# Performance work log

Hardware: AMD Instinct MI355X
Metric: run time of the kernel (lower is better)

The kernel has to match this reference:

```python
import jax, jax.numpy as jnp
import numpy as np

B, S, DIN, DOUT, H = 4, 2048, 512, 512, 8
DH = DOUT // H
EPS = 1e-5


def _conv_bn(x, conv_w, conv_b, bn_gamma, bn_beta, bn_mean, bn_var):
    # x: [B, S, DIN] -> permute to [B, DIN, S] like torch
    xc = jnp.transpose(x, (0, 2, 1))
    y = jax.lax.conv_general_dilated(
        xc, conv_w, window_strides=(1,), padding=[(3, 3)],
        dimension_numbers=('NCH', 'OIH', 'NCH'))  # [B, DOUT, S]
    y = y + conv_b[None, :, None]
    # BatchNorm1d in eval mode: normalize per channel with running stats
    inv = jax.lax.rsqrt(bn_var + EPS)
    y = (y - bn_mean[None, :, None]) * (inv * bn_gamma)[None, :, None] + bn_beta[None, :, None]
    return jnp.transpose(y, (0, 2, 1))  # back to [B, S, DOUT]


def setup_inputs() -> dict:
    key = jax.random.key(0)
    ks = jax.random.split(key, 4)
    return {
        'q': jax.random.normal(ks[0], (B, S, DIN), dtype=jnp.float32),
        'k': jax.random.normal(ks[1], (B, S, DIN), dtype=jnp.float32),
        'v': jax.random.normal(ks[2], (B, S, DIN), dtype=jnp.float32),
        'conv_w': jax.random.normal(ks[3], (DOUT, DIN, 7), dtype=jnp.float32) * 0.02,
        'conv_b': jnp.zeros((DOUT,), jnp.float32),
        'bn_gamma': jnp.ones((DOUT,), jnp.float32),
        'bn_beta': jnp.zeros((DOUT,), jnp.float32),
        'bn_mean': jnp.zeros((DOUT,), jnp.float32),
        'bn_var': jnp.ones((DOUT,), jnp.float32),
        'ln_gamma': jnp.ones((DOUT,), jnp.float32),
        'ln_beta': jnp.zeros((DOUT,), jnp.float32),
    }


def reference(q, k, v, conv_w, conv_b, bn_gamma, bn_beta, bn_mean, bn_var,
              ln_gamma, ln_beta):
    # shared conv+BN preproc applied to q, k, v, then split into heads [B,S,H,DH]
    qh = _conv_bn(q, conv_w, conv_b, bn_gamma, bn_beta, bn_mean, bn_var).reshape(B, S, H, DH)
    kh = _conv_bn(k, conv_w, conv_b, bn_gamma, bn_beta, bn_mean, bn_var).reshape(B, S, H, DH)
    vh = _conv_bn(v, conv_w, conv_b, bn_gamma, bn_beta, bn_mean, bn_var).reshape(B, S, H, DH)
    # full QK^T score matrix, scaled, softmax, times V (mask is None)
    scores = jnp.einsum('bqhd,bkhd->bhqk', qh, kh) * (1.0 / np.sqrt(DH).astype(np.float32))
    probs = jax.nn.softmax(scores, axis=-1)
    out = jnp.einsum('bhqk,bkhd->bqhd', probs, vh).reshape(B, S, DOUT)
    # dropout(p=0) is identity; final LayerNorm over feature dim
    mu = jnp.mean(out, axis=-1, keepdims=True)
    var = jnp.mean(jnp.square(out - mu), axis=-1, keepdims=True)
    return (out - mu) * jax.lax.rsqrt(var + EPS) * ln_gamma + ln_beta
```

## Files before the change

kernel.cpp:

```cpp
#include <hip/hip_runtime.h>
#include <hip/hip_bf16.h>


#define B_ 4
#define S_ 2048
#define DIN_ 512
#define DOUT_ 512
#define H_ 8
#define DH_ 64
#define EPS_ 1e-5f
#define SP_ 2054

using bf16x8 = __attribute__((ext_vector_type(8))) short;
using f32x4  = __attribute__((ext_vector_type(4))) float;

__device__ __forceinline__ unsigned short f2bf(float x) {
    union { float f; unsigned u; } v; v.f = x;
    unsigned r = v.u + 0x7FFF + ((v.u >> 16) & 1);
    return (unsigned short)(r >> 16);
}

__device__ __forceinline__ unsigned cvt2(float lo, float hi) {
    unsigned r;
    asm("v_cvt_pk_bf16_f32 %0, %1, %2" : "=v"(r) : "v"(lo), "v"(hi));
    return r;
}

__device__ __forceinline__ float fexp2(float x) {
    float r;
    asm("v_exp_f32 %0, %1" : "=v"(r) : "v"(x));
    return r;
}

__device__ __forceinline__ float bf2f(unsigned short u) {
    union { unsigned u; float f; } v; v.u = ((unsigned)u) << 16;
    return v.f;
}

typedef __attribute__((address_space(1))) const unsigned int GU32;
typedef __attribute__((address_space(3))) unsigned int LU32;
__device__ __forceinline__ void gl_lds16(const void* g, void* l) {
    __builtin_amdgcn_global_load_lds((GU32*)g, (LU32*)l, 16, 0, 0);
}

__global__ void cast_x(const float* __restrict__ q, const float* __restrict__ k,
                       const float* __restrict__ v, unsigned short* __restrict__ xb) {
    int i = blockIdx.x * 256 + threadIdx.x;
    int row = i >> 6;
    int cin = (i & 63) * 8;
    int tb = row / SP_;
    int pr = row - tb * SP_;
    int tensor = tb >> 2;
    int b = tb & 3;
    unsigned short* dst = xb + (size_t)row * DIN_ + cin;
    if (pr < 3 || pr >= SP_ - 3) {
        *reinterpret_cast<uint4*>(dst) = make_uint4(0, 0, 0, 0);
    } else {
        const float* src = (tensor == 0 ? q : (tensor == 1 ? k : v)) +
                           ((size_t)b * S_ + (pr - 3)) * DIN_ + cin;
        float4 a0 = *reinterpret_cast<const float4*>(src);
        float4 a1 = *reinterpret_cast<const float4*>(src + 4);
        uint4 o;
        o.x = cvt2(a0.x, a0.y); o.y = cvt2(a0.z, a0.w);
        o.z = cvt2(a1.x, a1.y); o.w = cvt2(a1.z, a1.w);
        *reinterpret_cast<uint4*>(dst) = o;
    }
}

__global__ void prep_w(const float* __restrict__ w, const float* __restrict__ cb,
                       const float* __restrict__ gamma, const float* __restrict__ beta,
                       const float* __restrict__ mean, const float* __restrict__ var,
                       unsigned short* __restrict__ w_eff, float* __restrict__ b_eff) {
    int gid = blockIdx.x * blockDim.x + threadIdx.x;
    if (gid < DOUT_) {
        float sc = gamma[gid] * rsqrtf(var[gid] + EPS_);
        b_eff[gid] = (cb[gid] - mean[gid]) * sc + beta[gid];
    }
    int total = 7 * DOUT_ * DIN_;
    for (int i = gid; i < total; i += gridDim.x * blockDim.x) {
        int t = i / (DOUT_ * DIN_);
        int rem = i - t * (DOUT_ * DIN_);
        int co = rem >> 9;
        int ci = rem & 511;
        float sc = gamma[co] * rsqrtf(var[co] + EPS_);
        w_eff[i] = f2bf(w[(co * DIN_ + ci) * 7 + t] * sc);
    }
}

__global__ __launch_bounds__(256, 3) void conv_bn(
        const unsigned short* __restrict__ xb,
        const unsigned short* __restrict__ w_eff,
        const float* __restrict__ b_eff,
        unsigned short* __restrict__ out3) {
    __shared__ alignas(16) unsigned short As[2][192 * 32];
    __shared__ alignas(16) unsigned short Bs[3][128 * 32];

    int orig = blockIdx.x;
    int bid = (orig & 7) * 96 + (orig >> 3);
    int tensor = bid >> 8;
    int rem = bid & 255;
    int batch = rem >> 6;
    int stile = (rem >> 2) & 15;
    int cotile = rem & 3;
    int s0 = stile * 128;
    int co0 = cotile * 128;

    const unsigned short* xp = xb + (size_t)(tensor * 4 + batch) * SP_ * DIN_;
    unsigned short* out = out3 + (size_t)tensor * (B_ * S_ * DOUT_) +
                          (size_t)batch * S_ * DOUT_;

    const int tid = threadIdx.x;
    const int l = tid & 63;
    const int wv = tid >> 6;
    const int g = l >> 4;
    const int c16 = l & 15;
    const int wrow = (wv >> 1) * 64;
    const int wcol = (wv & 1) * 64;

    const int dr4 = l >> 2;
    const int sch = ((l & 3) ^ ((l >> 3) & 3)) << 3;

#define STAGE_A(cc, buf) do {                                                   \
        _Pragma("unroll")                                                       \
        for (int j = 0; j < 3; ++j) {                                           \
            int r0 = (wv * 3 + j) * 16;                                         \
            int rs = r0 + dr4; if (rs > 133) rs = 133;                          \
            gl_lds16(xp + (size_t)(s0 + rs) * DIN_ + (cc) * 32 + sch,           \
                     &As[buf][r0 * 32]);                                        \
        }                                                                       \
    } while (0)

#define STAGE_B(cc, t, buf) do {                                                \
        const unsigned short* wp = w_eff + (size_t)(t) * (DOUT_ * DIN_) +       \
                                   (cc) * 32;                                   \
        _Pragma("unroll")                                                       \
        for (int j = 0; j < 2; ++j) {                                           \
            int r0 = (wv * 2 + j) * 16;                                         \
            gl_lds16(wp + (size_t)(co0 + r0 + dr4) * DIN_ + sch,                \
                     &Bs[buf][r0 * 32]);                                        \
        }                                                                       \
    } while (0)

    f32x4 acc[4][4] = {};

    STAGE_A(0, 0);
    STAGE_B(0, 0, 0);
    int bcur = 0;

    for (int cc = 0; cc < 16; ++cc) {
        const int ca = cc & 1;
        for (int t = 0; t < 7; ++t) {
            int bnext = (bcur == 2) ? 0 : bcur + 1;
            if (t < 6) {
                STAGE_B(cc, t + 1, bnext);
                asm volatile("s_waitcnt vmcnt(2)" ::: "memory");
            } else if (cc < 15) {
                STAGE_B(cc + 1, 0, bnext);
                STAGE_A(cc + 1, ca ^ 1);
                asm volatile("s_waitcnt vmcnt(5)" ::: "memory");
            } else {
                asm volatile("s_waitcnt vmcnt(0)" ::: "memory");
            }
            __builtin_amdgcn_s_barrier();

            const unsigned short* Ab = &As[ca][0];
            const unsigned short* Bb = &Bs[bcur][0];
            bf16x8 af[4], bfv[4];
#pragma unroll
            for (int m = 0; m < 4; ++m) {
                int r = wrow + m * 16 + c16 + t;
                af[m] = *reinterpret_cast<const bf16x8*>(
                    &Ab[r * 32 + ((g ^ ((r >> 1) & 3)) << 3)]);
            }
#pragma unroll
            for (int n = 0; n < 4; ++n) {
                int rb = wcol + n * 16 + c16;
                bfv[n] = *reinterpret_cast<const bf16x8*>(
                    &Bb[rb * 32 + ((g ^ ((rb >> 1) & 3)) << 3)]);
            }
            __builtin_amdgcn_s_setprio(1);
#pragma unroll
            for (int m = 0; m < 4; ++m)
#pragma unroll
                for (int n = 0; n < 4; ++n)
                    acc[m][n] = __builtin_amdgcn_mfma_f32_16x16x32_bf16(
                        af[m], bfv[n], acc[m][n], 0, 0, 0);
            __builtin_amdgcn_s_setprio(0);
            bcur = bnext;
        }
    }

    float osc = (tensor == 0) ? 0.125f * 1.44269504f : 1.0f;
#pragma unroll
    for (int m = 0; m < 4; ++m) {
        int rowb = s0 + wrow + m * 16 + 4 * g;
#pragma unroll
        for (int n = 0; n < 4; ++n) {
            int col = co0 + wcol + n * 16 + c16;
            float be = b_eff[col];
#pragma unroll
            for (int ri = 0; ri < 4; ++ri)
                out[(size_t)(rowb + ri) * DOUT_ + col] =
                    f2bf((acc[m][n][ri] + be) * osc);
        }
    }
#undef STAGE_A
#undef STAGE_B
}

__global__ void transpose_v(const unsigned short* __restrict__ vh,
                            unsigned short* __restrict__ vt) {
    __shared__ alignas(16) unsigned short T[64 * 64];
    int bid = blockIdx.x;
    int stile = bid & 31;
    int bh = bid >> 5;
    int b = bh >> 3;
    int h = bh & 7;
    int s0 = stile * 64;
    const unsigned short* src = vh + ((size_t)b * S_ + s0) * DOUT_ + h * DH_;
    unsigned short* dst = vt + (size_t)bh * DH_ * S_ + s0;
    int tid = threadIdx.x;
#pragma unroll
    for (int it = 0; it < 2; ++it) {
        int idx = tid + it * 256;
        int s = idx >> 3, dhc = idx & 7;
        uint4 val = *reinterpret_cast<const uint4*>(&src[(size_t)s * DOUT_ + dhc * 8]);
        *reinterpret_cast<uint4*>(&T[s * 64 + ((dhc ^ (s & 7) ^ ((s >> 3) & 7)) << 3)]) = val;
    }
    __syncthreads();
#pragma unroll
    for (int it = 0; it < 2; ++it) {
        int idx = tid + it * 256;
        int dh = idx >> 3, sc = idx & 7;
        unsigned short tmp[8];
#pragma unroll
        for (int j = 0; j < 8; ++j) {
            int s = sc * 8 + j;
            tmp[j] = T[s * 64 + (((dh >> 3) ^ (s & 7) ^ ((s >> 3) & 7)) << 3) + (dh & 7)];
        }
        *reinterpret_cast<uint4*>(&dst[(size_t)dh * S_ + sc * 8]) =
            *reinterpret_cast<const uint4*>(tmp);
    }
}

__global__ __launch_bounds__(256, 5) void attn(const unsigned short* __restrict__ qh,
                     const unsigned short* __restrict__ kh,
                     const unsigned short* __restrict__ vt,
                     unsigned short* __restrict__ part,
                     float2* __restrict__ ml) {
    __shared__ alignas(16) unsigned short Ks[2][64 * 64];
    __shared__ alignas(16) unsigned short Vs[2][64 * 64];

    const int tid = threadIdx.x;
    const int l = tid & 63;
    const int wv = tid >> 6;
    const int g = l >> 4;
    const int c16 = l & 15;

    const int bid = blockIdx.x;
    const int ks = bid >> 10;
    const int r10 = bid & 1023;
    const int qt = r10 & 31;
    const int bh = r10 >> 5;
    const int b = bh >> 3;
    const int h = bh & 7;
    const int s0 = qt * 64;

    const unsigned short* qp = qh + (size_t)b * S_ * DOUT_ + h * DH_;
    const unsigned short* kp = kh + (size_t)b * S_ * DOUT_ + h * DH_;
    const unsigned short* vp = vt + (size_t)bh * DH_ * S_;

    bf16x8 qf[2];
    {
        int row = s0 + wv * 16 + c16;
        qf[0] = *reinterpret_cast<const bf16x8*>(&qp[(size_t)row * DOUT_ + 8 * g]);
        qf[1] = *reinterpret_cast<const bf16x8*>(&qp[(size_t)row * DOUT_ + 32 + 8 * g]);
    }

    const int l3 = l >> 3;
    const int kchunk8 = ((l & 7) ^ l3) * 8;

#define STAGE(kt, buf) do {                                                          \
        const unsigned short* kgp = kp + (size_t)(kt) * 64 * DOUT_;                  \
        const unsigned short* vgp = vp + (size_t)(kt) * 64;                          \
        _Pragma("unroll")                                                            \
        for (int i = 0; i < 2; ++i) {                                                \
            int K0 = wv * 16 + i * 8;                                                \
            gl_lds16(kgp + (size_t)(K0 + l3) * DOUT_ + kchunk8, &Ks[buf][K0 * 64]);  \
            gl_lds16(vgp + (size_t)(K0 + l3) * S_   + kchunk8, &Vs[buf][K0 * 64]);   \
        }                                                                            \
    } while (0)

    f32x4 oacc[4] = {};
    float mrow = -1e30f, lrow = 0.f;

    const int sA = ((l & 16) << 1) | c16;
    const int sB = sA + 16;
    const bool hi = (l & 32) != 0;

    const int t0 = ks * 16;
    STAGE(t0, 0);

    for (int i = 0; i < 16; ++i) {
        const int cur = i & 1;
        if (i + 1 < 16) {
            STAGE(t0 + i + 1, 1 - cur);
            asm volatile("s_waitcnt vmcnt(4)" ::: "memory");
        } else {
            asm volatile("s_waitcnt vmcnt(0)" ::: "memory");
        }
        __builtin_amdgcn_s_barrier();

        const char* KsB = (const char*)&Ks[cur][0];
        f32x4 sf[4] = {};
#pragma unroll
        for (int kk = 0; kk < 2; ++kk) {
            bf16x8 kf[4];
#pragma unroll
            for (int n = 0; n < 4; ++n)
                kf[n] = *reinterpret_cast<const bf16x8*>(
                    KsB + (n * 16 + c16) * 128 + (((4 * kk + g) ^ (l & 7)) << 4));
            __builtin_amdgcn_s_setprio(1);
#pragma unroll
            for (int n = 0; n < 4; ++n)
                sf[n] = __builtin_amdgcn_mfma_f32_16x16x32_bf16(kf[n], qf[kk], sf[n], 0, 0, 0);
            __builtin_amdgcn_s_setprio(0);
        }

        float u0 = fmaxf(fmaxf(sf[0][0], sf[0][1]), fmaxf(sf[0][2], sf[0][3]));
        float u1 = fmaxf(fmaxf(sf[1][0], sf[1][1]), fmaxf(sf[1][2], sf[1][3]));
        float u2 = fmaxf(fmaxf(sf[2][0], sf[2][1]), fmaxf(sf[2][2], sf[2][3]));
        float u3 = fmaxf(fmaxf(sf[3][0], sf[3][1]), fmaxf(sf[3][2], sf[3][3]));
        float m0 = fmaxf(fmaxf(u0, u1), fmaxf(u2, u3));
        m0 = fmaxf(m0, __shfl_xor(m0, 16, 64));
        m0 = fmaxf(m0, __shfl_xor(m0, 32, 64));
        if (!__all(m0 <= mrow + 8.f)) {
            float mnew = fmaxf(mrow, m0);
            float corr = fexp2(mrow - mnew);
            mrow = mnew;
            lrow *= corr;
#pragma unroll
            for (int n = 0; n < 4; ++n) {
                oacc[n][0] *= corr; oacc[n][1] *= corr;
                oacc[n][2] *= corr; oacc[n][3] *= corr;
            }
        }
        unsigned pk[4][2];
        float rsn[4];
#pragma unroll
        for (int n = 0; n < 4; ++n) {
            float p0 = fexp2(sf[n][0] - mrow);
            float p1 = fexp2(sf[n][1] - mrow);
            float p2 = fexp2(sf[n][2] - mrow);
            float p3 = fexp2(sf[n][3] - mrow);
            rsn[n] = (p0 + p1) + (p2 + p3);
            pk[n][0] = cvt2(p0, p1);
            pk[n][1] = cvt2(p2, p3);
        }
        float rs = (rsn[0] + rsn[1]) + (rsn[2] + rsn[3]);
        rs += __shfl_xor(rs, 16, 64);
        rs += __shfl_xor(rs, 32, 64);
        lrow += rs;

        const char* VsB = (const char*)&Vs[cur][0];
#pragma unroll
        for (int kk = 0; kk < 2; ++kk) {
            unsigned a0 = __shfl((int)pk[2 * kk][0], sA, 64);
            unsigned a1 = __shfl((int)pk[2 * kk][1], sA, 64);
            unsigned a2 = __shfl((int)pk[2 * kk][0], sB, 64);
            unsigned a3 = __shfl((int)pk[2 * kk][1], sB, 64);
            unsigned b0 = __shfl((int)pk[2 * kk + 1][0], sA, 64);
            unsigned b1 = __shfl((int)pk[2 * kk + 1][1], sA, 64);
            unsigned b2 = __shfl((int)pk[2 * kk + 1][0], sB, 64);
            unsigned b3 = __shfl((int)pk[2 * kk + 1][1], sB, 64);
            union { unsigned w[4]; bf16x8 v; } pu;
            pu.w[0] = hi ? b0 : a0;
            pu.w[1] = hi ? b1 : a1;
            pu.w[2] = hi ? b2 : a2;
            pu.w[3] = hi ? b3 : a3;
            bf16x8 vfr[4];
#pragma unroll
            for (int n = 0; n < 4; ++n)
                vfr[n] = *reinterpret_cast<const bf16x8*>(
                    VsB + (n * 16 + c16) * 128 + (((4 * kk + g) ^ (l & 7)) << 4));
            __builtin_amdgcn_s_setprio(1);
#pragma unroll
            for (int n = 0; n < 4; ++n)
                oacc[n] = __builtin_amdgcn_mfma_f32_16x16x32_bf16(vfr[n], pu.v, oacc[n], 0, 0, 0);
            __builtin_amdgcn_s_setprio(0);
        }
        __builtin_amdgcn_s_barrier();
    }

    {
        int row = s0 + wv * 16 + c16;
        unsigned short* pp = part + (((size_t)ks * 32 + bh) * S_ + row) * DH_;
#pragma unroll
        for (int n = 0; n < 4; ++n) {
            uint2 w;
            w.x = cvt2(oacc[n][0], oacc[n][1]);
            w.y = cvt2(oacc[n][2], oacc[n][3]);
            *reinterpret_cast<uint2*>(&pp[n * 16 + 4 * g]) = w;
        }
        if (g == 0)
            ml[((size_t)ks * 32 + bh) * S_ + row] = make_float2(mrow, lrow);
    }
#undef STAGE
}

__global__ void combine_ln(const unsigned short* __restrict__ part,
                           const float2* __restrict__ ml,
                           const float* __restrict__ gamma,
                           const float* __restrict__ beta,
                           float* __restrict__ out) {
    int tid = threadIdx.x;
    int lane = tid & 63;
    int wv = tid >> 6;
    int row = blockIdx.x * 4 + wv;
    int b = row >> 11;
    int q = row & 2047;
    int h = lane >> 3;
    int dh0 = (lane & 7) * 8;

    size_t idx0 = ((size_t)(b * 8 + h)) * S_ + q;
    size_t idx1 = ((size_t)32 + b * 8 + h) * S_ + q;
    uint4 r0 = *reinterpret_cast<const uint4*>(&part[idx0 * DH_ + dh0]);
    uint4 r1 = *reinterpret_cast<const uint4*>(&part[idx1 * DH_ + dh0]);
    float2 ml0 = ml[idx0];
    float2 ml1 = ml[idx1];

    float m = fmaxf(ml0.x, ml1.x);
    float w0 = fexp2(ml0.x - m);
    float w1 = fexp2(ml1.x - m);
    float linv = 1.0f / (w0 * ml0.y + w1 * ml1.y);

    const unsigned short* e0 = reinterpret_cast<const unsigned short*>(&r0);
    const unsigned short* e1 = reinterpret_cast<const unsigned short*>(&r1);
    float o[8];
    float s = 0.f, sq = 0.f;
#pragma unroll
    for (int j = 0; j < 8; ++j) {
        float v = (w0 * bf2f(e0[j]) + w1 * bf2f(e1[j])) * linv;
        o[j] = v;
        s += v;
        sq += v * v;
    }
    for (int off = 1; off < 64; off <<= 1) {
        s += __shfl_xor(s, off, 64);
        sq += __shfl_xor(sq, off, 64);
    }
    float mu = s * (1.0f / 512.0f);
    float var = sq * (1.0f / 512.0f) - mu * mu;
    float rstd = rsqrtf(fmaxf(var, 0.f) + EPS_);

    int f0 = lane * 8;
    float4 g0 = *reinterpret_cast<const float4*>(&gamma[f0]);
    float4 g1 = *reinterpret_cast<const float4*>(&gamma[f0 + 4]);
    float4 b0 = *reinterpret_cast<const float4*>(&beta[f0]);
    float4 b1 = *reinterpret_cast<const float4*>(&beta[f0 + 4]);
    float4 o0, o1;
    o0.x = (o[0] - mu) * rstd * g0.x + b0.x;
    o0.y = (o[1] - mu) * rstd * g0.y + b0.y;
    o0.z = (o[2] - mu) * rstd * g0.z + b0.z;
    o0.w = (o[3] - mu) * rstd * g0.w + b0.w;
    o1.x = (o[4] - mu) * rstd * g1.x + b1.x;
    o1.y = (o[5] - mu) * rstd * g1.y + b1.y;
    o1.z = (o[6] - mu) * rstd * g1.z + b1.z;
    o1.w = (o[7] - mu) * rstd * g1.w + b1.w;
    float* op = out + (size_t)row * DOUT_ + f0;
    *reinterpret_cast<float4*>(op) = o0;
    *reinterpret_cast<float4*>(op + 4) = o1;
}

extern "C" void kernel_launch(void* const* d_in, const int* in_sizes, int n_in,
                              void* d_out, int out_size, void* d_ws, size_t ws_size,
                              hipStream_t stream) {
    const float* q        = (const float*)d_in[0];
    const float* k        = (const float*)d_in[1];
    const float* v        = (const float*)d_in[2];
    const float* conv_w   = (const float*)d_in[3];
    const float* conv_b   = (const float*)d_in[4];
    const float* bn_gamma = (const float*)d_in[5];
    const float* bn_beta  = (const float*)d_in[6];
    const float* bn_mean  = (const float*)d_in[7];
    const float* bn_var   = (const float*)d_in[8];
    const float* ln_gamma = (const float*)d_in[9];
    const float* ln_beta  = (const float*)d_in[10];

    unsigned short* qh    = (unsigned short*)d_ws;
    unsigned short* kh    = qh + (size_t)B_ * S_ * DOUT_;
    unsigned short* vh    = kh + (size_t)B_ * S_ * DOUT_;
    unsigned short* w_eff = vh + (size_t)B_ * S_ * DOUT_;
    float* b_eff          = (float*)(w_eff + (size_t)7 * DOUT_ * DIN_);
    unsigned short* xb    = (unsigned short*)(b_eff + DOUT_);
    unsigned short* vt    = xb;
    unsigned short* part  = xb + (size_t)12 * SP_ * DIN_;
    float2* ml            = (float2*)(part + (size_t)2 * B_ * H_ * S_ * DH_);

    float* out = (float*)d_out;

    cast_x<<<dim3(6162), dim3(256), 0, stream>>>(q, k, v, xb);
    prep_w<<<dim3(7168), dim3(256), 0, stream>>>(conv_w, conv_b, bn_gamma, bn_beta,
                                                 bn_mean, bn_var, w_eff, b_eff);
    conv_bn<<<dim3(768), dim3(256), 0, stream>>>(xb, w_eff, b_eff, qh);
    transpose_v<<<dim3(1024), dim3(256), 0, stream>>>(vh, vt);
    attn<<<dim3(2048), dim3(256), 0, stream>>>(qh, kh, vt, part, ml);
    combine_ln<<<dim3(2048), dim3(256), 0, stream>>>(part, ml, ln_gamma, ln_beta, out);
}
```

Measured before the change: 185.3 us.

## Process two 64-row query tiles per attention block to reuse staged K/V

Each attention block now handles 128 query rows (two independent groups per wave) instead of 64, so every K/V tile loaded into LDS feeds twice as many MFMAs. The grid is halved and launch bounds drop from 5 to 4 waves-per-EU to leave room for the doubled accumulators and softmax state. This cuts global/LDS traffic for K and V per query and interleaves two independent MFMA chains, at the cost of higher register pressure, lower occupancy and fewer blocks in the grid.

Measured after the change: 178.8 us, median of 2. -3.5%, faster.

```diff
diff --git a/kernel.cpp b/kernel.cpp
--- a/kernel.cpp
+++ b/kernel.cpp
@@ -243,7 +243,7 @@
     }
 }
 
-__global__ __launch_bounds__(256, 5) void attn(const unsigned short* __restrict__ qh,
+__global__ __launch_bounds__(256, 4) void attn(const unsigned short* __restrict__ qh,
                      const unsigned short* __restrict__ kh,
                      const unsigned short* __restrict__ vt,
                      unsigned short* __restrict__ part,
@@ -258,23 +258,26 @@
     const int c16 = l & 15;
 
     const int bid = blockIdx.x;
-    const int ks = bid >> 10;
-    const int r10 = bid & 1023;
-    const int qt = r10 & 31;
-    const int bh = r10 >> 5;
+    const int ks = bid >> 9;
+    const int r9 = bid & 511;
+    const int qt = r9 & 15;
+    const int bh = r9 >> 4;
     const int b = bh >> 3;
     const int h = bh & 7;
-    const int s0 = qt * 64;
+    const int s0 = qt * 128;
 
     const unsigned short* qp = qh + (size_t)b * S_ * DOUT_ + h * DH_;
     const unsigned short* kp = kh + (size_t)b * S_ * DOUT_ + h * DH_;
     const unsigned short* vp = vt + (size_t)bh * DH_ * S_;
 
-    bf16x8 qf[2];
+    bf16x8 qfA[2], qfB[2];
     {
-        int row = s0 + wv * 16 + c16;
-        qf[0] = *reinterpret_cast<const bf16x8*>(&qp[(size_t)row * DOUT_ + 8 * g]);
-        qf[1] = *reinterpret_cast<const bf16x8*>(&qp[(size_t)row * DOUT_ + 32 + 8 * g]);
+        int rowA = s0 + wv * 16 + c16;
+        int rowB = rowA + 64;
+        qfA[0] = *reinterpret_cast<const bf16x8*>(&qp[(size_t)rowA * DOUT_ + 8 * g]);
+        qfA[1] = *reinterpret_cast<const bf16x8*>(&qp[(size_t)rowA * DOUT_ + 32 + 8 * g]);
+        qfB[0] = *reinterpret_cast<const bf16x8*>(&qp[(size_t)rowB * DOUT_ + 8 * g]);
+        qfB[1] = *reinterpret_cast<const bf16x8*>(&qp[(size_t)rowB * DOUT_ + 32 + 8 * g]);
     }
 
     const int l3 = l >> 3;
@@ -291,8 +294,9 @@
         }                                                                            \
     } while (0)
 
-    f32x4 oacc[4] = {};
-    float mrow = -1e30f, lrow = 0.f;
+    f32x4 oaccA[4] = {}, oaccB[4] = {};
+    float mrowA = -1e30f, lrowA = 0.f;
+    float mrowB = -1e30f, lrowB = 0.f;
 
     const int sA = ((l & 16) << 1) | c16;
     const int sB = sA + 16;
@@ -300,6 +304,56 @@
 
     const int t0 = ks * 16;
     STAGE(t0, 0);
+
+#define SOFTMAX_GRP(sf, mrow, lrow, oacc, pk) do {                               \
+        float u0 = fmaxf(fmaxf(sf[0][0], sf[0][1]), fmaxf(sf[0][2], sf[0][3]));  \
+        float u1 = fmaxf(fmaxf(sf[1][0], sf[1][1]), fmaxf(sf[1][2], sf[1][3]));  \
+        float u2 = fmaxf(fmaxf(sf[2][0], sf[2][1]), fmaxf(sf[2][2], sf[2][3]));  \
+        float u3 = fmaxf(fmaxf(sf[3][0], sf[3][1]), fmaxf(sf[3][2], sf[3][3]));  \
+        float m0 = fmaxf(fmaxf(u0, u1), fmaxf(u2, u3));                          \
+        m0 = fmaxf(m0, __shfl_xor(m0, 16, 64));                                  \
+        m0 = fmaxf(m0, __shfl_xor(m0, 32, 64));                                  \
+        if (!__all(m0 <= mrow + 8.f)) {                                          \
+            float mnew = fmaxf(mrow, m0);                                        \
+            float corr = fexp2(mrow - mnew);                                     \
+            mrow = mnew;                                                         \
+            lrow *= corr;                                                        \
+            _Pragma("unroll")                                                    \
+            for (int n = 0; n < 4; ++n) {                                        \
+                oacc[n][0] *= corr; oacc[n][1] *= corr;                          \
+                oacc[n][2] *= corr; oacc[n][3] *= corr;                          \
+            }                                                                    \
+        }                                                                        \
+        float rsacc = 0.f;                                                       \
+        _Pragma("unroll")                                                        \
+        for (int n = 0; n < 4; ++n) {                                            \
+            float p0 = fexp2(sf[n][0] - mrow);                                   \
+            float p1 = fexp2(sf[n][1] - mrow);                                   \
+            float p2 = fexp2(sf[n][2] - mrow);                                   \
+            float p3 = fexp2(sf[n][3] - mrow);                                   \
+            rsacc += (p0 + p1) + (p2 + p3);                                      \
+            pk[n][0] = cvt2(p0, p1);                                             \
+            pk[n][1] = cvt2(p2, p3);                                             \
+        }                                                                        \
+        rsacc += __shfl_xor(rsacc, 16, 64);                                      \
+        rsacc += __shfl_xor(rsacc, 32, 64);                                      \
+        lrow += rsacc;                                                           \
+    } while (0)
+
+#define BUILD_PU(pk, kk, pu) do {                                                \
+        unsigned a0 = __shfl((int)pk[2 * (kk)][0], sA, 64);                      \
+        unsigned a1 = __shfl((int)pk[2 * (kk)][1], sA, 64);                      \
+        unsigned a2 = __shfl((int)pk[2 * (kk)][0], sB, 64);                      \
+        unsigned a3 = __shfl((int)pk[2 * (kk)][1], sB, 64);                      \
+        unsigned b0 = __shfl((int)pk[2 * (kk) + 1][0], sA, 64);                  \
+        unsigned b1 = __shfl((int)pk[2 * (kk) + 1][1], sA, 64);                  \
+        unsigned b2 = __shfl((int)pk[2 * (kk) + 1][0], sB, 64);                  \
+        unsigned b3 = __shfl((int)pk[2 * (kk) + 1][1], sB, 64);                  \
+        pu.w[0] = hi ? b0 : a0;                                                  \
+        pu.w[1] = hi ? b1 : a1;                                                  \
+        pu.w[2] = hi ? b2 : a2;                                                  \
+        pu.w[3] = hi ? b3 : a3;                                                  \
+    } while (0)
 
     for (int i = 0; i < 16; ++i) {
         const int cur = i & 1;
@@ -312,7 +366,7 @@
         __builtin_amdgcn_s_barrier();
 
         const char* KsB = (const char*)&Ks[cur][0];
-        f32x4 sf[4] = {};
+        f32x4 sfA[4] = {}, sfB[4] = {};
 #pragma unroll
         for (int kk = 0; kk < 2; ++kk) {
             bf16x8 kf[4];
@@ -322,62 +376,23 @@
                     KsB + (n * 16 + c16) * 128 + (((4 * kk + g) ^ (l & 7)) << 4));
             __builtin_amdgcn_s_setprio(1);
 #pragma unroll
-            for (int n = 0; n < 4; ++n)
-                sf[n] = __builtin_amdgcn_mfma_f32_16x16x32_bf16(kf[n], qf[kk], sf[n], 0, 0, 0);
+            for (int n = 0; n < 4; ++n) {
+                sfA[n] = __builtin_amdgcn_mfma_f32_16x16x32_bf16(kf[n], qfA[kk], sfA[n], 0, 0, 0);
+                sfB[n] = __builtin_amdgcn_mfma_f32_16x16x32_bf16(kf[n], qfB[kk], sfB[n], 0, 0, 0);
+            }
             __builtin_amdgcn_s_setprio(0);
         }
 
-        float u0 = fmaxf(fmaxf(sf[0][0], sf[0][1]), fmaxf(sf[0][2], sf[0][3]));
-        float u1 = fmaxf(fmaxf(sf[1][0], sf[1][1]), fmaxf(sf[1][2], sf[1][3]));
-        float u2 = fmaxf(fmaxf(sf[2][0], sf[2][1]), fmaxf(sf[2][2], sf[2][3]));
-        float u3 = fmaxf(fmaxf(sf[3][0], sf[3][1]), fmaxf(sf[3][2], sf[3][3]));
-        float m0 = fmaxf(fmaxf(u0, u1), fmaxf(u2, u3));
-        m0 = fmaxf(m0, __shfl_xor(m0, 16, 64));
-        m0 = fmaxf(m0, __shfl_xor(m0, 32, 64));
-        if (!__all(m0 <= mrow + 8.f)) {
-            float mnew = fmaxf(mrow, m0);
-            float corr = fexp2(mrow - mnew);
-            mrow = mnew;
-            lrow *= corr;
-#pragma unroll
-            for (int n = 0; n < 4; ++n) {
-                oacc[n][0] *= corr; oacc[n][1] *= corr;
-                oacc[n][2] *= corr; oacc[n][3] *= corr;
-            }
-        }
-        unsigned pk[4][2];
-        float rsn[4];
-#pragma unroll
-        for (int n = 0; n < 4; ++n) {
-            float p0 = fexp2(sf[n][0] - mrow);
-            float p1 = fexp2(sf[n][1] - mrow);
-            float p2 = fexp2(sf[n][2] - mrow);
-            float p3 = fexp2(sf[n][3] - mrow);
-            rsn[n] = (p0 + p1) + (p2 + p3);
-            pk[n][0] = cvt2(p0, p1);
-            pk[n][1] = cvt2(p2, p3);
-        }
-        float rs = (rsn[0] + rsn[1]) + (rsn[2] + rsn[3]);
-        rs += __shfl_xor(rs, 16, 64);
-        rs += __shfl_xor(rs, 32, 64);
-        lrow += rs;
+        unsigned pkA[4][2], pkB[4][2];
+        SOFTMAX_GRP(sfA, mrowA, lrowA, oaccA, pkA);
+        SOFTMAX_GRP(sfB, mrowB, lrowB, oaccB, pkB);
 
         const char* VsB = (const char*)&Vs[cur][0];
 #pragma unroll
         for (int kk = 0; kk < 2; ++kk) {
-            unsigned a0 = __shfl((int)pk[2 * kk][0], sA, 64);
-            unsigned a1 = __shfl((int)pk[2 * kk][1], sA, 64);
-            unsigned a2 = __shfl((int)pk[2 * kk][0], sB, 64);
-            unsigned a3 = __shfl((int)pk[2 * kk][1], sB, 64);
-            unsigned b0 = __shfl((int)pk[2 * kk + 1][0], sA, 64);
-            unsigned b1 = __shfl((int)pk[2 * kk + 1][1], sA, 64);
-            unsigned b2 = __shfl((int)pk[2 * kk + 1][0], sB, 64);
-            unsigned b3 = __shfl((int)pk[2 * kk + 1][1], sB, 64);
-            union { unsigned w[4]; bf16x8 v; } pu;
-            pu.w[0] = hi ? b0 : a0;
-            pu.w[1] = hi ? b1 : a1;
-            pu.w[2] = hi ? b2 : a2;
-            pu.w[3] = hi ? b3 : a3;
+            union { unsigned w[4]; bf16x8 v; } puA, puB;
+            BUILD_PU(pkA, kk, puA);
+            BUILD_PU(pkB, kk, puB);
             bf16x8 vfr[4];
 #pragma unroll
             for (int n = 0; n < 4; ++n)
@@ -385,27 +400,38 @@
                     VsB + (n * 16 + c16) * 128 + (((4 * kk + g) ^ (l & 7)) << 4));
             __builtin_amdgcn_s_setprio(1);
 #pragma unroll
-            for (int n = 0; n < 4; ++n)
-                oacc[n] = __builtin_amdgcn_mfma_f32_16x16x32_bf16(vfr[n], pu.v, oacc[n], 0, 0, 0);
+            for (int n = 0; n < 4; ++n) {
+                oaccA[n] = __builtin_amdgcn_mfma_f32_16x16x32_bf16(vfr[n], puA.v, oaccA[n], 0, 0, 0);
+                oaccB[n] = __builtin_amdgcn_mfma_f32_16x16x32_bf16(vfr[n], puB.v, oaccB[n], 0, 0, 0);
+            }
             __builtin_amdgcn_s_setprio(0);
         }
         __builtin_amdgcn_s_barrier();
     }
 
     {
-        int row = s0 + wv * 16 + c16;
-        unsigned short* pp = part + (((size_t)ks * 32 + bh) * S_ + row) * DH_;
+        int rowA = s0 + wv * 16 + c16;
+        int rowB = rowA + 64;
+        unsigned short* ppA = part + (((size_t)ks * 32 + bh) * S_ + rowA) * DH_;
+        unsigned short* ppB = part + (((size_t)ks * 32 + bh) * S_ + rowB) * DH_;
 #pragma unroll
         for (int n = 0; n < 4; ++n) {
-            uint2 w;
-            w.x = cvt2(oacc[n][0], oacc[n][1]);
-            w.y = cvt2(oacc[n][2], oacc[n][3]);
-            *reinterpret_cast<uint2*>(&pp[n * 16 + 4 * g]) = w;
-        }
-        if (g == 0)
-            ml[((size_t)ks * 32 + bh) * S_ + row] = make_float2(mrow, lrow);
+            uint2 wA, wB;
+            wA.x = cvt2(oaccA[n][0], oaccA[n][1]);
+            wA.y = cvt2(oaccA[n][2], oaccA[n][3]);
+            wB.x = cvt2(oaccB[n][0], oaccB[n][1]);
+            wB.y = cvt2(oaccB[n][2], oaccB[n][3]);
+            *reinterpret_cast<uint2*>(&ppA[n * 16 + 4 * g]) = wA;
+            *reinterpret_cast<uint2*>(&ppB[n * 16 + 4 * g]) = wB;
+        }
+        if (g == 0) {
+            ml[((size_t)ks * 32 + bh) * S_ + rowA] = make_float2(mrowA, lrowA);
+            ml[((size_t)ks * 32 + bh) * S_ + rowB] = make_float2(mrowB, lrowB);
+        }
     }
 #undef STAGE
+#undef SOFTMAX_GRP
+#undef BUILD_PU
 }
 
 __global__ void combine_ln(const unsigned short* __restrict__ part,
@@ -504,6 +530,6 @@
                                                  bn_mean, bn_var, w_eff, b_eff);
     conv_bn<<<dim3(768), dim3(256), 0, stream>>>(xb, w_eff, b_eff, qh);
     transpose_v<<<dim3(1024), dim3(256), 0, stream>>>(vh, vt);
-    attn<<<dim3(2048), dim3(256), 0, stream>>>(qh, kh, vt, part, ml);
+    attn<<<dim3(1024), dim3(256), 0, stream>>>(qh, kh, vt, part, ml);
     combine_ln<<<dim3(2048), dim3(256), 0, stream>>>(part, ml, ln_gamma, ln_beta, out);
 }
```
